# Optimization experiments

Measured on AMD Instinct MI355X. Metric: run time of the kernel, lower is better.

The kernel has to match this reference:

```python
import jax, jax.numpy as jnp
import numpy as np

# Module hyperparameters (from init_kwargs)
LEARNING_RATE = 0.01  # not used inside compute_weight_update
TAU_PLUS = 20.0
TAU_MINUS = 20.0
A_PLUS = 0.005
A_MINUS = 0.00525
TARGET_RATE = 0.1
HOMEOSTATIC_RATE = 0.001
TAU_HOMEOSTATIC = 1000.0

B, T, N_PRE, N_POST = 16, 8192, 128, 128


def setup_inputs() -> dict:
    key = jax.random.key(0)
    k1, k2, k3 = jax.random.split(key, 3)
    # Bernoulli spike trains at ~target_rate firing probability
    pre_spikes = (jax.random.uniform(k1, (B, T, N_PRE)) < TARGET_RATE).astype(jnp.float32)
    post_spikes = (jax.random.uniform(k2, (B, T, N_POST)) < TARGET_RATE).astype(jnp.float32)
    weights = jax.random.uniform(k3, (N_PRE, N_POST), dtype=jnp.float32)
    return {"pre_spikes": pre_spikes, "post_spikes": post_spikes, "weights": weights, "dt": 1}


def _temporal_corr(x, kernel, pad):
    """Correlate x [B,T,N] along time with 1-D kernel [L], padding pad=(lo,hi)."""
    b, t, n = x.shape
    xr = jnp.moveaxis(x, 1, 2).reshape(b * n, 1, t)  # [B*N, 1, T]
    k = kernel.reshape(1, 1, -1).astype(x.dtype)
    y = jax.lax.conv_general_dilated(
        xr, k, window_strides=(1,), padding=[pad],
        dimension_numbers=("NCH", "OIH", "NCH"))
    return jnp.moveaxis(y.reshape(b, n, t), 2, 1)  # [B,T,N]


def reference(pre_spikes, post_spikes, weights, dt):
    b, t, n_pre = pre_spikes.shape
    dt = float(dt)

    # Homeostatic rate tracking (first call: avg rates initialized to target_rate)
    alpha = dt / TAU_HOMEOSTATIC
    current_post_rate = post_spikes.mean(axis=(0, 1))
    avg_post_rate = (1.0 - alpha) * TARGET_RATE + alpha * current_post_rate

    # Truncated exponential STDP window: tau in 1..min(int(3*tau)-1, ...) = 1..59
    L = int(TAU_PLUS * 3)  # 60 taps (tau=0 tap zeroed)
    taus = jnp.arange(L, dtype=jnp.float32)
    w_plus = jnp.where(taus > 0, A_PLUS * jnp.exp(-taus * dt / TAU_PLUS), 0.0)
    w_minus = jnp.where(taus > 0, A_MINUS * jnp.exp(-taus * dt / TAU_MINUS), 0.0)

    # LTP: post_filt[t] = sum_{tau>=1} w_plus[tau] * post[t+tau] (future, zero-padded)
    post_filt = _temporal_corr(post_spikes, w_plus, (0, L - 1))
    # LTD: pre_filt[t] = sum_{tau>=1} w_minus[tau] * pre[t-tau] (past, zero-padded)
    pre_filt = _temporal_corr(pre_spikes, w_minus[::-1], (L - 1, 0))

    # sum_t mean_b outer(pre[t], post_filt[t]) - outer(pre_filt[t], post[t]), then /T
    ltp = jnp.einsum("btp,btq->pq", pre_spikes, post_filt)
    ltd = jnp.einsum("btp,btq->pq", pre_filt, post_spikes)
    stdp_update = (ltp - ltd) / (b * t)

    # Homeostatic regulation pulls post rate toward target
    post_rate_error = avg_post_rate - TARGET_RATE
    homeostatic_update = -HOMEOSTATIC_RATE * post_rate_error[None, :] * weights

    return stdp_update + homeostatic_update
```

## Files before the change

kernel.cpp:

```cpp
#include <hip/hip_runtime.h>

#define BB 16
#define TT 8192
#define NN 128
constexpr int CHUNK = 256;
constexpr int NBLK  = BB * TT / CHUNK;
constexpr int OUTN  = NN * NN;
constexpr int GS    = 260;
constexpr int SLOTS = OUTN / 2;
constexpr int NWAVE = 8;
constexpr int WIN   = CHUNK / NWAVE;

typedef _Float16 f16x8 __attribute__((ext_vector_type(8)));
typedef _Float16 f16x2 __attribute__((ext_vector_type(2)));
typedef float    f32x4 __attribute__((ext_vector_type(4)));

__device__ __forceinline__ unsigned short h16(float x) {
    _Float16 h = (_Float16)x;
    return __builtin_bit_cast(unsigned short, h);
}
__device__ __forceinline__ unsigned int pack2(float x, float y) {
    return (unsigned int)h16(x) | ((unsigned int)h16(y) << 16);
}

template<bool ATOMIC>
__global__ __launch_bounds__(512, 3)
void stdp_main(const float* __restrict__ pre, const float* __restrict__ post,
               const int* __restrict__ dtp,
               unsigned int* __restrict__ part, float* __restrict__ wpost,
               float* __restrict__ outat)
{
    __shared__ __align__(16) unsigned short bufG[NN * GS];
    __shared__ float lds_ps[NWAVE * NN];

    const int tid  = threadIdx.x;
    const int bi   = blockIdx.x;
    const int b    = bi >> 5;
    const int ch   = bi & 31;
    const int t00  = ch * CHUNK;
    const int wv   = tid >> 6;
    const int lane = tid & 63;

    const float dtf = (float)(*dtp);
    const float r   = expf(-dtf * (1.0f / 20.0f));

    const float* pb = post + (size_t)b * TT * NN;
    const float* ab = pre  + (size_t)b * TT * NN;

    const int q0   = lane * 2;
    const int base = wv * WIN;
    const float* prow = pb + (size_t)(t00 + 1) * NN + q0;
    const int mlim = TT - 2 - t00;

    float ps0 = 0.f, ps1 = 0.f;
    #define LDF(m) (*(const float2*)(prow + (size_t)(m) * NN))
    #define LDG(m) (((m) <= mlim) ? LDF(m) : make_float2(0.f, 0.f))
    #define FILTER_BODY(LD) {                                                 \
        const float r2 = r * r, r3 = r2 * r, r4 = r2 * r2;                    \
        float2 p = LD(base + 31);                                  \
        ps0 += p.x; ps1 += p.y;                                               \
        float gx0 = r  * p.x, gy0 = r  * p.y;                                 \
        p = LD(base + 32);                                         \
        float gx1 = r2 * p.x, gy1 = r2 * p.y;                                 \
        p = LD(base + 33);                                         \
        float gx2 = r3 * p.x, gy2 = r3 * p.y;                                 \
        p = LD(base + 34);                                         \
        float gx3 = r4 * p.x, gy3 = r4 * p.y;                                 \
        float wA = r * r4, wB = r2 * r4, wC = r3 * r4, wD = r4 * r4;          \
        _Pragma("unroll")                                                     \
        for (int j = 1; j < 15; ++j) {                                        \
            p = LD(base + 31 + 4 * j);                                        \
            gx0 = fmaf(wA, p.x, gx0); gy0 = fmaf(wA, p.y, gy0);               \
            p = LD(base + 32 + 4 * j);                                        \
            gx1 = fmaf(wB, p.x, gx1); gy1 = fmaf(wB, p.y, gy1);               \
            p = LD(base + 33 + 4 * j);                                        \
            gx2 = fmaf(wC, p.x, gx2); gy2 = fmaf(wC, p.y, gy2);               \
            if (j < 14) {                                                     \
                p = LD(base + 34 + 4 * j);                                    \
                gx3 = fmaf(wD, p.x, gx3); gy3 = fmaf(wD, p.y, gy3);           \
            }                                                                 \
            wA *= r4; wB *= r4; wC *= r4; wD *= r4;                           \
        }                                                                     \
        const float r8 = r4 * r4, r16 = r8 * r8, r32 = r16 * r16;             \
        const float r60 = ((r32 * r16) * r8) * r4;                            \
        float gx = (gx0 + gx1) + (gx2 + gx3);                                 \
        float gy = (gy0 + gy1) + (gy2 + gy3);                                 \
        float gkx = gx, gky = gy;                                  \
        unsigned short* d0 = &bufG[q0 * GS + base];                           \
        unsigned short* d1 = &bufG[(q0 + 1) * GS + base];                     \
        _Pragma("unroll")                                                     \
        for (int c = 30; c >= 0; --c) {                                       \
            const float2 p1  = LD(base + c);                                  \
            const float2 p60 = LD(base + c + 59);                             \
            gx = r * (gx + p1.x) - r60 * p60.x;                               \
            gy = r * (gy + p1.y) - r60 * p60.y;                               \
            ps0 += p1.x; ps1 += p1.y;                                         \
            if (c & 1) {                                                      \
                gkx = gx; gky = gy;                                           \
            } else {                                                          \
                *(unsigned int*)(d0 + c) = pack2(gx, gkx);                    \
                *(unsigned int*)(d1 + c) = pack2(gy, gky);                    \
            }                                                                 \
        }                                                                     \
    }

    if (base + 89 <= mlim) {
        FILTER_BODY(LDF)
    } else {
        FILTER_BODY(LDG)
    }

    lds_ps[wv * NN + q0]     = ps0;
    lds_ps[wv * NN + q0 + 1] = ps1;
    __syncthreads();

    if (tid < NN) {
        float s = 0.f;
        #pragma unroll
        for (int w = 0; w < NWAVE; ++w) s += lds_ps[w * NN + tid];
        if (ch == 0) s += pb[tid];
        if constexpr (ATOMIC) atomicAdd(&wpost[tid], s);
        else wpost[(size_t)bi * NN + tid] = s;
    }

    const int pr0 = wv * 16;
    f32x4 acc[8];
    #pragma unroll
    for (int qt = 0; qt < 8; ++qt) acc[qt] = (f32x4){0.f, 0.f, 0.f, 0.f};

    {
        const float* abase = ab + (size_t)(t00 + (lane >> 4) * 8) * NN + pr0 + (lane & 15);
        float an[8];
        #pragma unroll
        for (int j = 0; j < 8; ++j) an[j] = abase[(size_t)j * NN];
        #pragma unroll
        for (int ks = 0; ks < 8; ++ks) {
            f16x8 af;
            #pragma unroll
            for (int j = 0; j < 8; ++j) af[j] = (_Float16)an[j];
            if (ks < 7) {
                const float* src = abase + (size_t)((ks + 1) * 32) * NN;
                #pragma unroll
                for (int j = 0; j < 8; ++j) an[j] = src[(size_t)j * NN];
            }
            const int koff = ks * 32 + (lane >> 4) * 8;
            #pragma unroll
            for (int qt = 0; qt < 8; ++qt) {
                const unsigned short* gp = &bufG[(qt * 16 + (lane & 15)) * GS + koff];
                const uint2 lo = *(const uint2*)(gp);
                const uint2 hi = *(const uint2*)(gp + 4);
                const uint4 u  = make_uint4(lo.x, lo.y, hi.x, hi.y);
                const f16x8 bf = __builtin_bit_cast(f16x8, u);
                acc[qt] = __builtin_amdgcn_mfma_f32_16x16x32_f16(af, bf, acc[qt], 0, 0, 0);
            }
        }
    }

    if constexpr (!ATOMIC) {
        unsigned int* dst = part + ((size_t)bi * 8 + wv) * 1024 + lane;
        #pragma unroll
        for (int qt = 0; qt < 8; ++qt) {
            dst[qt * 128]      = pack2(acc[qt][0], acc[qt][1]);
            dst[qt * 128 + 64] = pack2(acc[qt][2], acc[qt][3]);
        }
    } else {
        #pragma unroll
        for (int qt = 0; qt < 8; ++qt)
            #pragma unroll
            for (int rg = 0; rg < 4; ++rg) {
                const int prow_o = pr0 + (lane >> 4) * 4 + rg;
                const int qcol   = qt * 16 + (lane & 15);
                atomicAdd(&outat[prow_o * NN + qcol], acc[qt][rg]);
            }
    }
    #undef FILTER_BODY
    #undef LDF
    #undef LDG
}

__global__ __launch_bounds__(512)
void finalize_ws(const unsigned int* __restrict__ part, const float* __restrict__ wpost,
                 const int* __restrict__ dtp, const float* __restrict__ W,
                 float* __restrict__ out)
{
    __shared__ float2 red[512];
    __shared__ float  hfs[16];
    const int s    = threadIdx.x & 63;
    const int kq   = threadIdx.x >> 6;
    const int slot = blockIdx.x * 64 + s;
    const int qt   = (slot >> 7) & 7;
    const int qbase = qt * 16;

    {
        const int qi = threadIdx.x >> 5;
        const int pr = threadIdx.x & 31;
        float hsum = 0.f;
        const int q = qbase + qi;
        #pragma unroll 4
        for (int k = pr; k < NBLK; k += 32) hsum += wpost[(size_t)k * NN + q];
        #pragma unroll
        for (int off = 16; off; off >>= 1) hsum += __shfl_down(hsum, off, 32);
        if (pr == 0) {
            const float dtf   = (float)(*dtp);
            const float alpha = dtf * 1e-3f;
            hfs[qi] = -0.001f * (alpha * (hsum * (1.0f / (float)(BB * TT)) - 0.1f));
        }
    }

    float sx = 0.f, sy = 0.f;
    #pragma unroll 8
    for (int k = kq * (NBLK / 8); k < (kq + 1) * (NBLK / 8); ++k) {
        const unsigned int v = part[(size_t)k * SLOTS + slot];
        const f16x2 h = __builtin_bit_cast(f16x2, v);
        sx += (float)h[0];
        sy += (float)h[1];
    }
    red[threadIdx.x] = make_float2(sx, sy);
    __syncthreads();
    if (threadIdx.x < 64) {
        float tx = red[s].x, ty = red[s].y;
        #pragma unroll
        for (int g = 1; g < 8; ++g) {
            const float2 v = red[g * 64 + s];
            tx += v.x; ty += v.y;
        }
        const int lane = slot & 63;
        const int rp   = (slot >> 6) & 1;
        const int wv   = slot >> 10;
        const int p    = wv * 16 + ((lane >> 4) << 2) + rp * 2;
        const int qi   = lane & 15;
        const int q    = qbase + qi;
        const float scale = (float)((0.005 - 0.00525) / (double)(BB * TT));
        const float hf = hfs[qi];
        out[p * NN + q]       = fmaf(tx, scale, hf * W[p * NN + q]);
        out[(p + 1) * NN + q] = fmaf(ty, scale, hf * W[(p + 1) * NN + q]);
    }
}

__global__ void finalize_at(const float* __restrict__ wpost, const int* __restrict__ dtp,
                            const float* __restrict__ W, float* __restrict__ out)
{
    const int i = (blockIdx.x * 256 + threadIdx.x) * 2;
    const int q = i & 127;
    const float scale = (float)((0.005 - 0.00525) / (double)(BB * TT));
    const float dtf   = (float)(*dtp);
    const float alpha = dtf * 1e-3f;
    const float inv   = 1.0f / (float)(BB * TT);
    const float hf0   = -0.001f * (alpha * (wpost[q]     * inv - 0.1f));
    const float hf1   = -0.001f * (alpha * (wpost[q + 1] * inv - 0.1f));
    float2 sv = *(const float2*)(out + i);
    float2 w  = *(const float2*)(W + i);
    float2 o;
    o.x = fmaf(sv.x, scale, hf0 * w.x);
    o.y = fmaf(sv.y, scale, hf1 * w.y);
    *(float2*)(out + i) = o;
}

extern "C" void kernel_launch(void* const* d_in, const int* in_sizes, int n_in,
                              void* d_out, int out_size, void* d_ws, size_t ws_size,
                              hipStream_t stream)
{
    const float* pre  = (const float*)d_in[0];
    const float* post = (const float*)d_in[1];
    const float* W    = (const float*)d_in[2];
    const int*   dtp  = (const int*)d_in[3];
    float* out = (float*)d_out;

    const size_t part_bytes  = (size_t)NBLK * SLOTS * sizeof(unsigned int);
    const size_t wpost_bytes = (size_t)NBLK * NN * sizeof(float);
    const size_t need = part_bytes + wpost_bytes;

    if (ws_size >= need) {
        unsigned int* part = (unsigned int*)d_ws;
        float* wpost       = (float*)((char*)d_ws + part_bytes);
        hipLaunchKernelGGL((stdp_main<false>), dim3(NBLK), dim3(512), 0, stream,
                           pre, post, dtp, part, wpost, (float*)nullptr);
        hipLaunchKernelGGL(finalize_ws, dim3(SLOTS / 64), dim3(512), 0, stream,
                           part, wpost, dtp, W, out);
    } else {
        float* wpost = (float*)d_ws;
        hipMemsetAsync(d_out, 0, OUTN * sizeof(float), stream);
        hipMemsetAsync(wpost, 0, NN * sizeof(float), stream);
        hipLaunchKernelGGL((stdp_main<true>), dim3(NBLK), dim3(512), 0, stream,
                           pre, post, dtp, (unsigned int*)nullptr, wpost, out);
        hipLaunchKernelGGL(finalize_at, dim3(OUTN / 512), dim3(256), 0, stream,
                           wpost, dtp, W, out);
    }
}
```

Measured before the change: 180.5 us.

## Compute temporal STDP filter with MFMA banded-Toeplitz matmuls instead of scalar recurrence

Replaces the per-lane scalar exponential filter (FMA warm-up plus a sliding recurrence) with a banded Toeplitz weight matrix held in f16 fragments and applied through MFMA 16x16x32 instructions. Each step produces a 16-timestep by 16-neuron tile of filtered post spikes that goes straight into LDS. The post-rate sum moves into a separate simple loop, and the launch-bounds occupancy hint drops from 3 to 2. The filter weights are now quantized to f16, and the MFMA path adds redundant zero-tap work in exchange for removing long serial FMA chains.

```diff
diff --git a/kernel.cpp b/kernel.cpp
--- a/kernel.cpp
+++ b/kernel.cpp
@@ -9,7 +9,6 @@
 constexpr int GS    = 260;
 constexpr int SLOTS = OUTN / 2;
 constexpr int NWAVE = 8;
-constexpr int WIN   = CHUNK / NWAVE;
 
 typedef _Float16 f16x8 __attribute__((ext_vector_type(8)));
 typedef _Float16 f16x2 __attribute__((ext_vector_type(2)));
@@ -24,7 +23,7 @@
 }
 
 template<bool ATOMIC>
-__global__ __launch_bounds__(512, 3)
+__global__ __launch_bounds__(512, 2)
 void stdp_main(const float* __restrict__ pre, const float* __restrict__ post,
                const int* __restrict__ dtp,
                unsigned int* __restrict__ part, float* __restrict__ wpost,
@@ -40,78 +39,89 @@
     const int t00  = ch * CHUNK;
     const int wv   = tid >> 6;
     const int lane = tid & 63;
+    const int cl   = lane & 15;
+    const int kg   = lane >> 4;
 
     const float dtf = (float)(*dtp);
-    const float r   = expf(-dtf * (1.0f / 20.0f));
+    const float lw  = -dtf * (1.0f / 20.0f);
 
     const float* pb = post + (size_t)b * TT * NN;
     const float* ab = pre  + (size_t)b * TT * NN;
 
-    const int q0   = lane * 2;
-    const int base = wv * WIN;
-    const float* prow = pb + (size_t)(t00 + 1) * NN + q0;
     const int mlim = TT - 2 - t00;
 
-    float ps0 = 0.f, ps1 = 0.f;
-    #define LDF(m) (*(const float2*)(prow + (size_t)(m) * NN))
-    #define LDG(m) (((m) <= mlim) ? LDF(m) : make_float2(0.f, 0.f))
-    #define FILTER_BODY(LD) {                                                 \
-        const float r2 = r * r, r3 = r2 * r, r4 = r2 * r2;                    \
-        float2 p = LD(base + 31);                                  \
-        ps0 += p.x; ps1 += p.y;                                               \
-        float gx0 = r  * p.x, gy0 = r  * p.y;                                 \
-        p = LD(base + 32);                                         \
-        float gx1 = r2 * p.x, gy1 = r2 * p.y;                                 \
-        p = LD(base + 33);                                         \
-        float gx2 = r3 * p.x, gy2 = r3 * p.y;                                 \
-        p = LD(base + 34);                                         \
-        float gx3 = r4 * p.x, gy3 = r4 * p.y;                                 \
-        float wA = r * r4, wB = r2 * r4, wC = r3 * r4, wD = r4 * r4;          \
-        _Pragma("unroll")                                                     \
-        for (int j = 1; j < 15; ++j) {                                        \
-            p = LD(base + 31 + 4 * j);                                        \
-            gx0 = fmaf(wA, p.x, gx0); gy0 = fmaf(wA, p.y, gy0);               \
-            p = LD(base + 32 + 4 * j);                                        \
-            gx1 = fmaf(wB, p.x, gx1); gy1 = fmaf(wB, p.y, gy1);               \
-            p = LD(base + 33 + 4 * j);                                        \
-            gx2 = fmaf(wC, p.x, gx2); gy2 = fmaf(wC, p.y, gy2);               \
-            if (j < 14) {                                                     \
-                p = LD(base + 34 + 4 * j);                                    \
-                gx3 = fmaf(wD, p.x, gx3); gy3 = fmaf(wD, p.y, gy3);           \
-            }                                                                 \
-            wA *= r4; wB *= r4; wC *= r4; wD *= r4;                           \
-        }                                                                     \
-        const float r8 = r4 * r4, r16 = r8 * r8, r32 = r16 * r16;             \
-        const float r60 = ((r32 * r16) * r8) * r4;                            \
-        float gx = (gx0 + gx1) + (gx2 + gx3);                                 \
-        float gy = (gy0 + gy1) + (gy2 + gy3);                                 \
-        float gkx = gx, gky = gy;                                  \
-        unsigned short* d0 = &bufG[q0 * GS + base];                           \
-        unsigned short* d1 = &bufG[(q0 + 1) * GS + base];                     \
-        _Pragma("unroll")                                                     \
-        for (int c = 30; c >= 0; --c) {                                       \
-            const float2 p1  = LD(base + c);                                  \
-            const float2 p60 = LD(base + c + 59);                             \
-            gx = r * (gx + p1.x) - r60 * p60.x;                               \
-            gy = r * (gy + p1.y) - r60 * p60.y;                               \
-            ps0 += p1.x; ps1 += p1.y;                                         \
-            if (c & 1) {                                                      \
-                gkx = gx; gky = gy;                                           \
-            } else {                                                          \
-                *(unsigned int*)(d0 + c) = pack2(gx, gkx);                    \
-                *(unsigned int*)(d1 + c) = pack2(gy, gky);                    \
+    f16x8 wf[6];
+    #pragma unroll
+    for (int vi = 0; vi < 6; ++vi) {
+        const int V = vi * 16 - 16;
+        #pragma unroll
+        for (int j = 0; j < 8; ++j) {
+            const int d = V + kg * 8 + j - cl;
+            wf[vi][j] = (d >= 0 && d <= 58) ? (_Float16)__expf(lw * (float)(d + 1))
+                                            : (_Float16)0.0f;
+        }
+    }
+
+    const int qb = wv * 16;
+    const float* pbase = pb + (size_t)(t00 + 1) * NN + qb + cl;
+
+    #define LOADFRAG(dstf, M) {                                               \
+        const float* p0_ = pbase + (size_t)((M) + kg * 8) * NN;               \
+        if ((M) + 31 <= mlim) {                                               \
+            _Pragma("unroll")                                                 \
+            for (int j = 0; j < 8; ++j) dstf[j] = (_Float16)p0_[(size_t)j * NN]; \
+        } else {                                                              \
+            _Pragma("unroll")                                                 \
+            for (int j = 0; j < 8; ++j) {                                     \
+                const int m_ = (M) + kg * 8 + j;                              \
+                dstf[j] = (m_ <= mlim) ? (_Float16)p0_[(size_t)j * NN]        \
+                                       : (_Float16)0.0f;                      \
             }                                                                 \
         }                                                                     \
     }
 
-    if (base + 89 <= mlim) {
-        FILTER_BODY(LDF)
-    } else {
-        FILTER_BODY(LDG)
-    }
-
-    lds_ps[wv * NN + q0]     = ps0;
-    lds_ps[wv * NN + q0 + 1] = ps1;
+    {
+        f16x8 fr0, fr1, fr2;
+        LOADFRAG(fr0, 0)
+        LOADFRAG(fr1, 32)
+        LOADFRAG(fr2, 64)
+        #pragma unroll
+        for (int s = 0; s < 16; ++s) {
+            const int tb = s * 16;
+            if (s >= 2 && (s & 1) == 0) {
+                fr0 = fr1; fr1 = fr2;
+                LOADFRAG(fr2, tb + 64)
+            }
+            f32x4 g = (f32x4){0.f, 0.f, 0.f, 0.f};
+            if (s & 1) {
+                g = __builtin_amdgcn_mfma_f32_16x16x32_f16(wf[0], fr0, g, 0, 0, 0);
+                g = __builtin_amdgcn_mfma_f32_16x16x32_f16(wf[2], fr1, g, 0, 0, 0);
+                g = __builtin_amdgcn_mfma_f32_16x16x32_f16(wf[4], fr2, g, 0, 0, 0);
+            } else {
+                g = __builtin_amdgcn_mfma_f32_16x16x32_f16(wf[1], fr0, g, 0, 0, 0);
+                g = __builtin_amdgcn_mfma_f32_16x16x32_f16(wf[3], fr1, g, 0, 0, 0);
+                g = __builtin_amdgcn_mfma_f32_16x16x32_f16(wf[5], fr2, g, 0, 0, 0);
+            }
+            *(uint2*)&bufG[(qb + cl) * GS + tb + kg * 4] =
+                make_uint2(pack2(g[0], g[1]), pack2(g[2], g[3]));
+        }
+    }
+    #undef LOADFRAG
+
+    {
+        float ps0 = 0.f, ps1 = 0.f;
+        const float* pr2 = pb + (size_t)(t00 + 1) * NN + lane * 2;
+        #pragma unroll
+        for (int i = 0; i < 32; ++i) {
+            const int m = wv * 32 + i;
+            if (ch != 31 || m <= mlim) {
+                const float2 v = *(const float2*)(pr2 + (size_t)m * NN);
+                ps0 += v.x; ps1 += v.y;
+            }
+        }
+        lds_ps[wv * NN + lane * 2]     = ps0;
+        lds_ps[wv * NN + lane * 2 + 1] = ps1;
+    }
     __syncthreads();
 
     if (tid < NN) {
@@ -129,7 +139,7 @@
     for (int qt = 0; qt < 8; ++qt) acc[qt] = (f32x4){0.f, 0.f, 0.f, 0.f};
 
     {
-        const float* abase = ab + (size_t)(t00 + (lane >> 4) * 8) * NN + pr0 + (lane & 15);
+        const float* abase = ab + (size_t)(t00 + kg * 8) * NN + pr0 + cl;
         float an[8];
         #pragma unroll
         for (int j = 0; j < 8; ++j) an[j] = abase[(size_t)j * NN];
@@ -143,10 +153,10 @@
                 #pragma unroll
                 for (int j = 0; j < 8; ++j) an[j] = src[(size_t)j * NN];
             }
-            const int koff = ks * 32 + (lane >> 4) * 8;
+            const int koff = ks * 32 + kg * 8;
             #pragma unroll
             for (int qt = 0; qt < 8; ++qt) {
-                const unsigned short* gp = &bufG[(qt * 16 + (lane & 15)) * GS + koff];
+                const unsigned short* gp = &bufG[(qt * 16 + cl) * GS + koff];
                 const uint2 lo = *(const uint2*)(gp);
                 const uint2 hi = *(const uint2*)(gp + 4);
                 const uint4 u  = make_uint4(lo.x, lo.y, hi.x, hi.y);
@@ -168,14 +178,11 @@
         for (int qt = 0; qt < 8; ++qt)
             #pragma unroll
             for (int rg = 0; rg < 4; ++rg) {
-                const int prow_o = pr0 + (lane >> 4) * 4 + rg;
-                const int qcol   = qt * 16 + (lane & 15);
+                const int prow_o = pr0 + kg * 4 + rg;
+                const int qcol   = qt * 16 + cl;
                 atomicAdd(&outat[prow_o * NN + qcol], acc[qt][rg]);
             }
     }
-    #undef FILTER_BODY
-    #undef LDF
-    #undef LDG
 }
 
 __global__ __launch_bounds__(512)
```

After: 170.6 us. 1.06x faster.
